# Performance work log

Measured on AMD Instinct MI355X. Metric: run time of the kernel, lower is better.

Reference implementation:

```python
import jax, jax.numpy as jnp
import numpy as np


def setup_inputs() -> dict:
    key = jax.random.key(0)
    k1, k2, k3 = jax.random.split(key, 3)
    B, F, P, T = 8, 128, 256, 2048
    return {
        "flashes_pe": jax.random.uniform(k1, (B, F, P), dtype=jnp.float32),
        "flashes_time": jax.random.uniform(k2, (B, F, 1), dtype=jnp.float32),
        "flashes_confidence": jax.random.uniform(k3, (B, F, 1), dtype=jnp.float32),
        "num_ticks": T,
        "sigma": jnp.float32(1.0),
    }


def reference(flashes_pe, flashes_time, flashes_confidence, num_ticks, sigma):
    # flashes_pe: [B, F, P], flashes_time/confidence: [B, F, 1]
    # time bin center per flash, clamped to valid tick range -> [B, F]
    time_bins = jnp.clip(flashes_time * num_ticks, 0.0, num_ticks - 1)[..., 0]
    ticks = jnp.arange(num_ticks, dtype=flashes_pe.dtype)  # [T]
    # Gaussian soft binning weights over ticks -> [B, F, T]
    z = (ticks[None, None, :] - time_bins[..., None]) / sigma
    w = jnp.exp(-0.5 * z * z)
    w = w / (w.sum(axis=2, keepdims=True) + 1e-10)
    # confidence-scaled PE -> [B, F, P]
    scaled_pe = flashes_pe * flashes_confidence
    # sum of outer products over flashes; avoids materializing [B,F,P,T]
    waveform = jnp.einsum("bfp,bft->bpt", scaled_pe, w)  # [B, P, T]
    return waveform
```

## Files before the change

### kernel.cpp

```cpp
#include <hip/hip_runtime.h>


#define F       128
#define TT      32
#define BLOCK   256
#define MAXSLOT 128
#define CHUNK   8

__global__ __launch_bounds__(BLOCK) void flash_reco_tile(
    const float* __restrict__ pe,
    const float* __restrict__ ftime,
    const float* __restrict__ fconf,
    const float* __restrict__ sig_p,
    float* __restrict__ out,
    int P, int T, int ntiles)
{
    __shared__ int   wcnt[4];
    __shared__ int   fl_f [MAXSLOT];
    __shared__ float fl_tb[MAXSLOT];
    __shared__ float fl_sc[MAXSLOT];
    __shared__ int   fl_lo[MAXSLOT];
    __shared__ int   fl_len[MAXSLOT];
    __shared__ float wt[MAXSLOT * TT];

    const int tid  = threadIdx.x;
    const int b    = blockIdx.x / ntiles;
    const int tile = blockIdx.x % ntiles;
    const int t0   = tile * TT;
    const float sigma   = *sig_p;
    const float inv_sig = 1.0f / sigma;

    bool act = false;
    float tb = 0.f, cf = 0.f;
    int lo = 0, len = 0;
    if (tid < F) {
        const float tm = ftime[b * F + tid];
        cf = fconf[b * F + tid];
        tb = fminf(fmaxf(tm * (float)T, 0.0f), (float)(T - 1));
        const float r = 8.0f * sigma;
        lo = (int)ceilf(tb - r);       if (lo < 0) lo = 0;
        int hi = (int)floorf(tb + r);  if (hi > T - 1) hi = T - 1;
        len = hi - lo + 1;
        act = (lo <= t0 + TT - 1) && (hi >= t0);
    }
    const unsigned long long m = __ballot(act);
    const int lane = tid & 63, wv = tid >> 6;
    if (lane == 0) wcnt[wv] = __popcll(m);
    __syncthreads();
    const int count = wcnt[0] + wcnt[1];
    if (act) {
        const int slot = __popcll(m & ((1ULL << lane) - 1ULL))
                       + (wv == 1 ? wcnt[0] : 0);
        fl_f[slot]  = tid;
        fl_tb[slot] = tb;
        fl_sc[slot] = cf;
        fl_lo[slot] = lo;
        fl_len[slot] = len;
    }
    __syncthreads();

    float sv[CHUNK];
    #pragma unroll
    for (int u = 0; u < CHUNK; ++u)
        sv[u] = (u < count) ? pe[((long)b * F + fl_f[u]) * P + tid] : 0.0f;

    for (int idx = tid; idx < count * TT; idx += BLOCK) {
        const int a = idx >> 5, j = idx & (TT - 1);
        const float z = ((float)(t0 + j) - fl_tb[a]) * inv_sig;
        wt[idx] = __expf(-0.5f * z * z);
    }
    for (int a = tid; a < count; a += BLOCK) {
        const float tbv = fl_tb[a];
        const int lov = fl_lo[a], lenv = fl_len[a];
        float s = 0.0f;
        for (int k = 0; k < lenv; ++k) {
            const float z = ((float)(lov + k) - tbv) * inv_sig;
            s += __expf(-0.5f * z * z);
        }
        fl_sc[a] = fl_sc[a] / (s + 1e-10f);
    }
    __syncthreads();

    float acc[TT];
    #pragma unroll
    for (int j = 0; j < TT; ++j) acc[j] = 0.0f;

    #pragma unroll
    for (int a = 0; a < CHUNK; ++a) {
        if (a < count) {
            const float s = sv[a] * fl_sc[a];
            const float4* w4 = (const float4*)&wt[a * TT];
            #pragma unroll
            for (int q = 0; q < TT / 4; ++q) {
                const float4 w = w4[q];
                acc[q*4+0] += s * w.x;
                acc[q*4+1] += s * w.y;
                acc[q*4+2] += s * w.z;
                acc[q*4+3] += s * w.w;
            }
        }
    }
    for (int a = CHUNK; a < count; ++a) {
        const float s = pe[((long)b * F + fl_f[a]) * P + tid] * fl_sc[a];
        const float4* w4 = (const float4*)&wt[a * TT];
        #pragma unroll
        for (int q = 0; q < TT / 4; ++q) {
            const float4 w = w4[q];
            acc[q*4+0] += s * w.x;
            acc[q*4+1] += s * w.y;
            acc[q*4+2] += s * w.z;
            acc[q*4+3] += s * w.w;
        }
    }

    float4* o4 = (float4*)(out + (long)b * P * T + (long)tid * T + t0);
    #pragma unroll
    for (int q = 0; q < TT / 4; ++q)
        o4[q] = make_float4(acc[q*4+0], acc[q*4+1], acc[q*4+2], acc[q*4+3]);
}

extern "C" void kernel_launch(void* const* d_in, const int* in_sizes, int n_in,
                              void* d_out, int out_size, void* d_ws, size_t ws_size,
                              hipStream_t stream) {
    const float* pe    = (const float*)d_in[0];
    const float* ftime = (const float*)d_in[1];
    const float* fconf = (const float*)d_in[2];
    const float* sigma = (const float*)d_in[4];

    const int BF = in_sizes[1];
    const int P  = in_sizes[0] / BF;
    const int B  = BF / F;
    const int T  = out_size / (B * P);
    const int ntiles = (T + TT - 1) / TT;

    flash_reco_tile<<<dim3(B * ntiles), dim3(BLOCK), 0, stream>>>(
        pe, ftime, fconf, sigma, (float*)d_out, P, T, ntiles);
}
```

Baseline: 14.87 us.

## Use closed-form Gaussian normalizer and coalesce output stores via LDS staging

Replaces the per-flash discrete Gaussian normalization loop with a closed-form approximation (a Jacobi theta expansion) when sigma is large enough and the flash window lies away from the boundaries, keeping the explicit sum as a fallback. The normalizer is now computed in the initial per-flash pass, so the separate serialized normalization loop after weight generation goes away. Output is staged through padded shared memory so each warp writes contiguous 128-byte row segments with nontemporal vector stores, replacing the earlier per-thread row-strided float4 stores. This costs an extra barrier and roughly 33KB more LDS, which may lower occupancy. The approximation slightly changes numerics.

```diff
diff --git a/kernel.cpp b/kernel.cpp
--- a/kernel.cpp
+++ b/kernel.cpp
@@ -7,6 +7,8 @@
 #define MAXSLOT 128
 #define CHUNK   8
 
+typedef float fvec4 __attribute__((ext_vector_type(4)));
+
 __global__ __launch_bounds__(BLOCK) void flash_reco_tile(
     const float* __restrict__ pe,
     const float* __restrict__ ftime,
@@ -15,13 +17,12 @@
     float* __restrict__ out,
     int P, int T, int ntiles)
 {
-    __shared__ int   wcnt[4];
+    __shared__ int   wcnt[2];
     __shared__ int   fl_f [MAXSLOT];
     __shared__ float fl_tb[MAXSLOT];
     __shared__ float fl_sc[MAXSLOT];
-    __shared__ int   fl_lo[MAXSLOT];
-    __shared__ int   fl_len[MAXSLOT];
-    __shared__ float wt[MAXSLOT * TT];
+    __shared__ float wt [MAXSLOT * TT];
+    __shared__ float stg[BLOCK * (TT + 1)];
 
     const int tid  = threadIdx.x;
     const int b    = blockIdx.x / ntiles;
@@ -29,23 +30,38 @@
     const int t0   = tile * TT;
     const float sigma   = *sig_p;
     const float inv_sig = 1.0f / sigma;
+    const float r       = 8.0f * sigma;
 
     bool act = false;
-    float tb = 0.f, cf = 0.f;
-    int lo = 0, len = 0;
+    float tb = 0.f, sc = 0.f;
     if (tid < F) {
         const float tm = ftime[b * F + tid];
-        cf = fconf[b * F + tid];
+        const float cf = fconf[b * F + tid];
         tb = fminf(fmaxf(tm * (float)T, 0.0f), (float)(T - 1));
-        const float r = 8.0f * sigma;
-        lo = (int)ceilf(tb - r);       if (lo < 0) lo = 0;
-        int hi = (int)floorf(tb + r);  if (hi > T - 1) hi = T - 1;
-        len = hi - lo + 1;
-        act = (lo <= t0 + TT - 1) && (hi >= t0);
+        act = (tb + r >= (float)t0) && (tb - r <= (float)(t0 + TT - 1));
+        if (act) {
+            float denom;
+            if (sigma >= 0.6f && tb - r > 0.0f && tb + r < (float)(T - 1)) {
+                const float q  = __expf(-19.7392088f * sigma * sigma);
+                const float fr = tb - truncf(tb);
+                denom = sigma * 2.50662827f
+                      * (1.0f + 2.0f * q * __cosf(6.28318531f * fr));
+            } else {
+                int lo = (int)ceilf(tb - r);   if (lo < 0) lo = 0;
+                int hi = (int)floorf(tb + r);  if (hi > T - 1) hi = T - 1;
+                float s = 0.0f;
+                for (int k = lo; k <= hi; ++k) {
+                    const float z = ((float)k - tb) * inv_sig;
+                    s += __expf(-0.5f * z * z);
+                }
+                denom = s;
+            }
+            sc = cf / (denom + 1e-10f);
+        }
     }
     const unsigned long long m = __ballot(act);
     const int lane = tid & 63, wv = tid >> 6;
-    if (lane == 0) wcnt[wv] = __popcll(m);
+    if (wv < 2 && lane == 0) wcnt[wv] = __popcll(m);
     __syncthreads();
     const int count = wcnt[0] + wcnt[1];
     if (act) {
@@ -53,9 +69,7 @@
                        + (wv == 1 ? wcnt[0] : 0);
         fl_f[slot]  = tid;
         fl_tb[slot] = tb;
-        fl_sc[slot] = cf;
-        fl_lo[slot] = lo;
-        fl_len[slot] = len;
+        fl_sc[slot] = sc;
     }
     __syncthreads();
 
@@ -68,16 +82,6 @@
         const int a = idx >> 5, j = idx & (TT - 1);
         const float z = ((float)(t0 + j) - fl_tb[a]) * inv_sig;
         wt[idx] = __expf(-0.5f * z * z);
-    }
-    for (int a = tid; a < count; a += BLOCK) {
-        const float tbv = fl_tb[a];
-        const int lov = fl_lo[a], lenv = fl_len[a];
-        float s = 0.0f;
-        for (int k = 0; k < lenv; ++k) {
-            const float z = ((float)(lov + k) - tbv) * inv_sig;
-            s += __expf(-0.5f * z * z);
-        }
-        fl_sc[a] = fl_sc[a] / (s + 1e-10f);
     }
     __syncthreads();
 
@@ -113,10 +117,23 @@
         }
     }
 
-    float4* o4 = (float4*)(out + (long)b * P * T + (long)tid * T + t0);
     #pragma unroll
-    for (int q = 0; q < TT / 4; ++q)
-        o4[q] = make_float4(acc[q*4+0], acc[q*4+1], acc[q*4+2], acc[q*4+3]);
+    for (int j = 0; j < TT; ++j)
+        stg[tid * (TT + 1) + j] = acc[j];
+    __syncthreads();
+
+    const long rowbase = (long)b * P * T + t0;
+    #pragma unroll
+    for (int g = 0; g < BLOCK / 32; ++g) {
+        const int p  = g * 32 + (tid >> 3);
+        const int j4 = (tid & 7) * 4;
+        fvec4 v;
+        v.x = stg[p * (TT + 1) + j4 + 0];
+        v.y = stg[p * (TT + 1) + j4 + 1];
+        v.z = stg[p * (TT + 1) + j4 + 2];
+        v.w = stg[p * (TT + 1) + j4 + 3];
+        __builtin_nontemporal_store(v, (fvec4*)(out + rowbase + (long)p * T + j4));
+    }
 }
 
 extern "C" void kernel_launch(void* const* d_in, const int* in_sizes, int n_in,
```

New measurement: 17.72 us. 19.2% more time.
